# Kernel optimization log

Hardware: AMD Instinct MI355X
Metric: run time of the kernel (lower is better)

## Reference

```python
import jax, jax.numpy as jnp
import numpy as np
from jax import lax

VOCAB, NUM_CLASSES = 21128, 53
EMB, FILT, K = 128, 128, 3
B, L = 512, 512


def setup_inputs() -> dict:
    key = jax.random.key(0)
    ks = jax.random.split(key, 8)
    char_ids = jax.random.randint(ks[0], (B, L), 0, VOCAB, dtype=jnp.int64 if jax.config.jax_enable_x64 else jnp.int32)
    pos_e1 = jax.random.randint(ks[1], (B,), 0, L - 1, dtype=jnp.int32)
    pos_e2 = jax.random.randint(ks[2], (B,), 0, L - 1, dtype=jnp.int32)
    emb_table = jax.random.normal(ks[3], (VOCAB, EMB), dtype=jnp.float32) * 0.02
    emb_table = emb_table.at[0].set(0.0)  # padding_idx=0
    conv_w = jax.random.normal(ks[4], (FILT, EMB, K), dtype=jnp.float32) * (1.0 / np.sqrt(EMB * K))
    conv_b = jax.random.normal(ks[5], (FILT,), dtype=jnp.float32) * 0.01
    fc_w = jax.random.normal(ks[6], (NUM_CLASSES, FILT * 3), dtype=jnp.float32) * (1.0 / np.sqrt(FILT * 3))
    fc_b = jax.random.normal(ks[7], (NUM_CLASSES,), dtype=jnp.float32) * 0.01
    return {"char_ids": char_ids, "pos_e1": pos_e1, "pos_e2": pos_e2,
            "emb_table": emb_table, "conv_w": conv_w, "conv_b": conv_b,
            "fc_w": fc_w, "fc_b": fc_b}


def reference(char_ids, pos_e1, pos_e2, emb_table, conv_w, conv_b, fc_w, fc_b):
    b, seq = char_ids.shape
    x = emb_table[char_ids]                      # (b, L, E)
    x = jnp.transpose(x, (0, 2, 1))              # (b, E, L)
    conv_out = lax.conv_general_dilated(
        x, conv_w, window_strides=(1,), padding=[(K // 2, K // 2)],
        dimension_numbers=("NCH", "OIH", "NCH"))
    conv_out = jax.nn.relu(conv_out + conv_b[None, :, None])  # (b, F, L)

    # sort + clip entity boundaries, replicate e1==e2 -> e2=e1+1 adjustment
    e1 = jnp.clip(jnp.minimum(pos_e1, pos_e2), 0, seq)
    e2 = jnp.clip(jnp.maximum(pos_e1, pos_e2), 0, seq)
    e2 = jnp.where(e1 == e2, jnp.minimum(e1 + 1, seq), e2)

    idx = jnp.arange(seq)[None, :]               # (1, L)
    m1 = idx < jnp.maximum(e1, 1)[:, None]       # [:e1] or [:1] if e1==0
    m2 = (idx >= e1[:, None]) & (idx < e2[:, None])
    m3 = idx >= jnp.minimum(e2, seq - 1)[:, None]  # [e2:] or last col if e2==L

    neg = jnp.float32(-jnp.inf)
    def seg_max(mask):
        return jnp.max(jnp.where(mask[:, None, :], conv_out, neg), axis=-1)  # (b, F)

    pooled = jnp.concatenate([seg_max(m1), seg_max(m2), seg_max(m3)], axis=-1)  # (b, 3F)
    return pooled @ fc_w.T + fc_b
```

## Files before the change

### kernel.cpp

```cpp
#include <hip/hip_runtime.h>
#include <stdint.h>

#define VOCAB 21128
#define NUMC  53
#define EMB   128
#define SEQ   512
#define BATCH 512

typedef __bf16 bf16x8 __attribute__((ext_vector_type(8)));
typedef float f32x4 __attribute__((ext_vector_type(4)));
typedef __attribute__((address_space(3))) void lds_void;
typedef const __attribute__((address_space(1))) void glob_void;

__device__ __forceinline__ unsigned int f2bf1(float f) {
    union { float f; unsigned int u; } v; v.f = f;
    return (v.u + 0x7FFFu + ((v.u >> 16) & 1u)) >> 16;
}
__device__ __forceinline__ unsigned int pack2(float a, float b) {
    return f2bf1(a) | (f2bf1(b) << 16);
}

__global__ void prep_kernel(const float* __restrict__ emb, const float* __restrict__ cw,
                            unsigned short* __restrict__ Tb, unsigned short* __restrict__ Wp) {
    int idx = blockIdx.x * blockDim.x + threadIdx.x;
    const int n8 = VOCAB * EMB / 8;
    if (idx < n8) {
        const float4* src = (const float4*)emb + (size_t)idx * 2;
        float4 a = src[0], b = src[1];
        uint4 o;
        o.x = pack2(a.x, a.y);
        o.y = pack2(a.z, a.w);
        o.z = pack2(b.x, b.y);
        o.w = pack2(b.z, b.w);
        *(uint4*)(Tb + (size_t)idx * 8) = o;
    }
    if (idx < 12 * 8 * 64 * 8) {
        int j = idx & 7, l = (idx >> 3) & 63, g = (idx >> 9) & 7, s = idx >> 12;
        int kk = s * 32 + (l >> 4) * 8 + j;
        int f = g * 16 + (l & 15);
        int tap = kk >> 7, e = kk & 127;
        Wp[idx] = (unsigned short)f2bf1(cw[(f * EMB + e) * 3 + tap]);
    }
}

__launch_bounds__(256, 6)
__global__ void pcnn_tile(const int* __restrict__ cid, const int* __restrict__ p1,
                          const int* __restrict__ p2,
                          const unsigned short* __restrict__ Tb,
                          const unsigned short* __restrict__ Wp,
                          float* __restrict__ Pd) {
    __shared__ __align__(16) unsigned short xs[66 * 128];

    const int bx   = blockIdx.x;
    const int b    = bx >> 3;
    const int tq   = bx & 7;
    const int tid  = threadIdx.x;
    const int lane = tid & 63;
    const int wn   = tid >> 6;
    const int quad = lane >> 4;
    const int lc   = lane & 15;

    const int* crow = cid + (size_t)b * SEQ;
    const char* TbB = (const char*)Tb;
    char* xsB = (char*)xs;

#pragma unroll
    for (int i = 0; i < 5; ++i) {
        int task = tid + 256 * i;
        if (task < 1056) {
            int r = task >> 4, c = task & 15;
            int p = tq * 64 + r - 1;
            unsigned int id = (p >= 0 && p < SEQ) ? (unsigned int)crow[p] : 0u;
            int cs = c ^ (r & 15);
            __builtin_amdgcn_global_load_lds(
                (glob_void*)(TbB + (size_t)id * 256u + cs * 16),
                (lds_void*)(xsB + task * 16), 16, 0, 0);
        }
    }

    int e1 = min(p1[b], p2[b]);
    int e2 = max(p1[b], p2[b]);
    if (e1 == e2) e2 = min(e1 + 1, SEQ);
    const int e1m = max(e1, 1);

    __syncthreads();

    f32x4 acc[4][2];
#pragma unroll
    for (int mt = 0; mt < 4; ++mt)
#pragma unroll
        for (int nt = 0; nt < 2; ++nt)
            acc[mt][nt] = (f32x4){0.f, 0.f, 0.f, 0.f};

#pragma unroll
    for (int s = 0; s < 12; ++s) {
        const int tap = s >> 2;
        const int q   = (s & 3) * 4 + quad;
        const int cs  = q ^ ((lc + tap) & 15);
        bf16x8 b0 = *(const bf16x8*)(Wp + (size_t)((s * 8 + wn * 2) * 64 + lane) * 8);
        bf16x8 b1 = *(const bf16x8*)(Wp + (size_t)((s * 8 + wn * 2 + 1) * 64 + lane) * 8);
#pragma unroll
        for (int mt = 0; mt < 4; ++mt) {
            int r = mt * 16 + lc + tap;
            bf16x8 a = *(const bf16x8*)(xs + r * 128 + cs * 8);
            acc[mt][0] = __builtin_amdgcn_mfma_f32_16x16x32_bf16(a, b0, acc[mt][0], 0, 0, 0);
            acc[mt][1] = __builtin_amdgcn_mfma_f32_16x16x32_bf16(a, b1, acc[mt][1], 0, 0, 0);
        }
    }

    float smax[3][2];
#pragma unroll
    for (int s3 = 0; s3 < 3; ++s3) { smax[s3][0] = -1e30f; smax[s3][1] = -1e30f; }

#pragma unroll
    for (int mt = 0; mt < 4; ++mt)
#pragma unroll
        for (int reg = 0; reg < 4; ++reg) {
            int p = tq * 64 + mt * 16 + quad * 4 + reg;
            float a0 = (p < e1m) ? 0.f : -2e30f;
            float a1 = (p >= e1 && p < e2) ? 0.f : -2e30f;
            float a2 = (p >= e2) ? 0.f : -2e30f;
#pragma unroll
            for (int nt = 0; nt < 2; ++nt) {
                float v = acc[mt][nt][reg];
                smax[0][nt] = fmaxf(smax[0][nt], v + a0);
                smax[1][nt] = fmaxf(smax[1][nt], v + a1);
                smax[2][nt] = fmaxf(smax[2][nt], v + a2);
            }
        }

#pragma unroll
    for (int s3 = 0; s3 < 3; ++s3)
#pragma unroll
        for (int nt = 0; nt < 2; ++nt) {
            float v = smax[s3][nt];
            v = fmaxf(v, __shfl_xor(v, 16));
            v = fmaxf(v, __shfl_xor(v, 32));
            smax[s3][nt] = v;
        }
    if (lane < 16) {
        float* pd = Pd + ((size_t)b * 8 + tq) * 384;
#pragma unroll
        for (int s3 = 0; s3 < 3; ++s3)
#pragma unroll
            for (int nt = 0; nt < 2; ++nt)
                pd[s3 * 128 + wn * 32 + nt * 16 + lc] = smax[s3][nt];
    }
}

__launch_bounds__(256)
__global__ void pcnn_combine(const float* __restrict__ Pd, const float* __restrict__ cb,
                             const float* __restrict__ fcw, const float* __restrict__ fcb,
                             float* __restrict__ out) {
    __shared__ float pooled[384];
    __shared__ float fcred[NUMC][4];
    const int b = blockIdx.x;
    const int tid = threadIdx.x;

    for (int j = tid; j < 384; j += 256) {
        const float* pp = Pd + (size_t)b * 8 * 384 + j;
        float m0 = fmaxf(pp[0 * 384], pp[1 * 384]);
        float m1 = fmaxf(pp[2 * 384], pp[3 * 384]);
        float m2 = fmaxf(pp[4 * 384], pp[5 * 384]);
        float m3 = fmaxf(pp[6 * 384], pp[7 * 384]);
        float m = fmaxf(fmaxf(m0, m1), fmaxf(m2, m3));
        pooled[j] = fmaxf(m + cb[j & 127], 0.f);
    }
    __syncthreads();

    if (tid < 212) {
        int c = tid >> 2, q = tid & 3;
        const float* wrow = fcw + (size_t)c * 384 + q * 96;
        const float* pp   = pooled + q * 96;
        float sum = 0.f;
#pragma unroll 8
        for (int i = 0; i < 96; ++i) sum += wrow[i] * pp[i];
        fcred[c][q] = sum;
    }
    __syncthreads();
    if (tid < NUMC)
        out[(size_t)b * NUMC + tid] =
            fcred[tid][0] + fcred[tid][1] + fcred[tid][2] + fcred[tid][3] + fcb[tid];
}

extern "C" void kernel_launch(void* const* d_in, const int* in_sizes, int n_in,
                              void* d_out, int out_size, void* d_ws, size_t ws_size,
                              hipStream_t stream) {
    const int*   cid = (const int*)d_in[0];
    const int*   p1  = (const int*)d_in[1];
    const int*   p2  = (const int*)d_in[2];
    const float* emb = (const float*)d_in[3];
    const float* cw  = (const float*)d_in[4];
    const float* cb  = (const float*)d_in[5];
    const float* fcw = (const float*)d_in[6];
    const float* fcb = (const float*)d_in[7];
    float* out = (float*)d_out;

    unsigned short* Tb = (unsigned short*)d_ws;
    unsigned short* Wp = (unsigned short*)((char*)d_ws + (size_t)VOCAB * EMB * 2);
    float*          Pd = (float*)((char*)d_ws + (size_t)VOCAB * EMB * 2 + 98304);

    const int n8 = VOCAB * EMB / 8;
    const int prep_threads = 256;
    const int prep_blocks  = (n8 + prep_threads - 1) / prep_threads;
    prep_kernel<<<prep_blocks, prep_threads, 0, stream>>>(emb, cw, Tb, Wp);
    pcnn_tile<<<BATCH * 8, 256, 0, stream>>>(cid, p1, p2, Tb, Wp, Pd);
    pcnn_combine<<<BATCH, 256, 0, stream>>>(Pd, cb, fcw, fcb, out);
}
```

Baseline: 114.9 us.

## Fuse embedding bf16 conversion into tile kernel, drop full-table prep pass

```diff
diff --git a/kernel.cpp b/kernel.cpp
--- a/kernel.cpp
+++ b/kernel.cpp
@@ -9,8 +9,6 @@
 
 typedef __bf16 bf16x8 __attribute__((ext_vector_type(8)));
 typedef float f32x4 __attribute__((ext_vector_type(4)));
-typedef __attribute__((address_space(3))) void lds_void;
-typedef const __attribute__((address_space(1))) void glob_void;
 
 __device__ __forceinline__ unsigned int f2bf1(float f) {
     union { float f; unsigned int u; } v; v.f = f;
@@ -20,20 +18,8 @@
     return f2bf1(a) | (f2bf1(b) << 16);
 }
 
-__global__ void prep_kernel(const float* __restrict__ emb, const float* __restrict__ cw,
-                            unsigned short* __restrict__ Tb, unsigned short* __restrict__ Wp) {
+__global__ void prep_kernel(const float* __restrict__ cw, unsigned short* __restrict__ Wp) {
     int idx = blockIdx.x * blockDim.x + threadIdx.x;
-    const int n8 = VOCAB * EMB / 8;
-    if (idx < n8) {
-        const float4* src = (const float4*)emb + (size_t)idx * 2;
-        float4 a = src[0], b = src[1];
-        uint4 o;
-        o.x = pack2(a.x, a.y);
-        o.y = pack2(a.z, a.w);
-        o.z = pack2(b.x, b.y);
-        o.w = pack2(b.z, b.w);
-        *(uint4*)(Tb + (size_t)idx * 8) = o;
-    }
     if (idx < 12 * 8 * 64 * 8) {
         int j = idx & 7, l = (idx >> 3) & 63, g = (idx >> 9) & 7, s = idx >> 12;
         int kk = s * 32 + (l >> 4) * 8 + j;
@@ -43,10 +29,10 @@
     }
 }
 
-__launch_bounds__(256, 6)
+__launch_bounds__(256, 4)
 __global__ void pcnn_tile(const int* __restrict__ cid, const int* __restrict__ p1,
                           const int* __restrict__ p2,
-                          const unsigned short* __restrict__ Tb,
+                          const float* __restrict__ emb,
                           const unsigned short* __restrict__ Wp,
                           float* __restrict__ Pd) {
     __shared__ __align__(16) unsigned short xs[66 * 128];
@@ -61,20 +47,31 @@
     const int lc   = lane & 15;
 
     const int* crow = cid + (size_t)b * SEQ;
-    const char* TbB = (const char*)Tb;
-    char* xsB = (char*)xs;
-
+
+    float4 ga[5], gb[5];
 #pragma unroll
     for (int i = 0; i < 5; ++i) {
         int task = tid + 256 * i;
-        if (task < 1056) {
+        if (i < 4 || tid < 32) {
             int r = task >> 4, c = task & 15;
             int p = tq * 64 + r - 1;
             unsigned int id = (p >= 0 && p < SEQ) ? (unsigned int)crow[p] : 0u;
             int cs = c ^ (r & 15);
-            __builtin_amdgcn_global_load_lds(
-                (glob_void*)(TbB + (size_t)id * 256u + cs * 16),
-                (lds_void*)(xsB + task * 16), 16, 0, 0);
+            const float4* src = (const float4*)(emb + (size_t)id * EMB + cs * 8);
+            ga[i] = src[0];
+            gb[i] = src[1];
+        }
+    }
+#pragma unroll
+    for (int i = 0; i < 5; ++i) {
+        int task = tid + 256 * i;
+        if (i < 4 || tid < 32) {
+            uint4 o;
+            o.x = pack2(ga[i].x, ga[i].y);
+            o.y = pack2(ga[i].z, ga[i].w);
+            o.z = pack2(gb[i].x, gb[i].y);
+            o.w = pack2(gb[i].z, gb[i].w);
+            *(uint4*)((char*)xs + task * 16) = o;
         }
     }
 
@@ -196,14 +193,10 @@
     const float* fcb = (const float*)d_in[7];
     float* out = (float*)d_out;
 
-    unsigned short* Tb = (unsigned short*)d_ws;
-    unsigned short* Wp = (unsigned short*)((char*)d_ws + (size_t)VOCAB * EMB * 2);
-    float*          Pd = (float*)((char*)d_ws + (size_t)VOCAB * EMB * 2 + 98304);
-
-    const int n8 = VOCAB * EMB / 8;
-    const int prep_threads = 256;
-    const int prep_blocks  = (n8 + prep_threads - 1) / prep_threads;
-    prep_kernel<<<prep_blocks, prep_threads, 0, stream>>>(emb, cw, Tb, Wp);
-    pcnn_tile<<<BATCH * 8, 256, 0, stream>>>(cid, p1, p2, Tb, Wp, Pd);
+    unsigned short* Wp = (unsigned short*)d_ws;
+    float*          Pd = (float*)((char*)d_ws + 98304);
+
+    prep_kernel<<<192, 256, 0, stream>>>(cw, Wp);
+    pcnn_tile<<<BATCH * 8, 256, 0, stream>>>(cid, p1, p2, emb, Wp, Pd);
     pcnn_combine<<<BATCH, 256, 0, stream>>>(Pd, cb, fcw, fcb, out);
 }
```

Result: slower. 120.2 us (+4.5%).
